# Performance work log

Measured on AMD Instinct MI355X. Metric: run time of the kernel, lower is better.

The kernel has to match this reference:

```python
import jax, jax.numpy as jnp
import numpy as np

D_MODEL = 1024
NUM_HEADS = 16
D_K = D_MODEL // NUM_HEADS


def setup_inputs() -> dict:
    key = jax.random.key(0)
    ks = jax.random.split(key, 5)
    B, S = 4, 2048
    scale = 1.0 / np.sqrt(D_MODEL)
    x = jax.random.normal(ks[0], (B, S, D_MODEL), dtype=jnp.float32)
    # Linear(d_model, d_model, bias=False) weights, stored as [out, in] like torch
    Wq = jax.random.normal(ks[1], (D_MODEL, D_MODEL), dtype=jnp.float32) * scale
    Wk = jax.random.normal(ks[2], (D_MODEL, D_MODEL), dtype=jnp.float32) * scale
    Wv = jax.random.normal(ks[3], (D_MODEL, D_MODEL), dtype=jnp.float32) * scale
    Wo = jax.random.normal(ks[4], (D_MODEL, D_MODEL), dtype=jnp.float32) * scale
    return {"x": x, "Wq": Wq, "Wk": Wk, "Wv": Wv, "Wo": Wo}


def reference(x, Wq, Wk, Wv, Wo):
    B, S, D = x.shape
    H, dk = NUM_HEADS, D_K
    # projections (torch Linear: x @ W.T)
    q = (x @ Wq.T).reshape(B, S, H, dk).transpose(0, 2, 1, 3)  # [B,H,S,dk]
    k = (x @ Wk.T).reshape(B, S, H, dk).transpose(0, 2, 1, 3)
    v = (x @ Wv.T).reshape(B, S, H, dk).transpose(0, 2, 1, 3)
    scores = jnp.einsum("bhqd,bhkd->bhqk", q, k) / jnp.sqrt(jnp.float32(dk))
    causal = jnp.triu(jnp.ones((S, S), dtype=bool), k=1)  # True above diagonal -> masked
    scores = jnp.where(causal[None, None], -jnp.inf, scores)
    attn = jax.nn.softmax(scores, axis=-1)
    out = jnp.einsum("bhqk,bhkd->bhqd", attn, v)  # [B,H,S,dk]
    out = out.transpose(0, 2, 1, 3).reshape(B, S, D)
    return out @ Wo.T
```

## Files before the change

kernel.cpp:

```cpp
#include <hip/hip_runtime.h>

typedef __bf16 bf16_t;
typedef __bf16 bf16x8 __attribute__((ext_vector_type(8)));
typedef __bf16 bf16x4 __attribute__((ext_vector_type(4)));
typedef float f32x4 __attribute__((ext_vector_type(4)));
typedef unsigned short u16x8 __attribute__((ext_vector_type(8)));

#define AS1C(p) ((const __attribute__((address_space(1))) void*)(p))
#define AS3(p) ((__attribute__((address_space(3))) void*)(p))

__device__ __forceinline__ unsigned short f2b_rne(float f) {
  union { float f; unsigned u; } x; x.f = f;
  unsigned u = x.u;
  u += 0x7fffu + ((u >> 16) & 1u);
  return (unsigned short)(u >> 16);
}

__global__ __launch_bounds__(256) void cast_f32_bf16(const float* __restrict__ in,
                                                     unsigned short* __restrict__ out,
                                                     int n) {
  int i = (blockIdx.x * 256 + threadIdx.x) * 8;
  if (i >= n) return;
  const float4* p = reinterpret_cast<const float4*>(in + i);
  float4 a = p[0], b = p[1];
  u16x8 o;
  o[0] = f2b_rne(a.x); o[1] = f2b_rne(a.y); o[2] = f2b_rne(a.z); o[3] = f2b_rne(a.w);
  o[4] = f2b_rne(b.x); o[5] = f2b_rne(b.y); o[6] = f2b_rne(b.z); o[7] = f2b_rne(b.w);
  *reinterpret_cast<u16x8*>(out + i) = o;
}

template <int OUT_F32>
__global__ __launch_bounds__(256) void gemm_bt(const bf16_t* __restrict__ A,
                                               const bf16_t* __restrict__ Bm,
                                               void* __restrict__ C,
                                               int M, int N, int K, int lda,
                                               float scale, int qlim) {
  __shared__ bf16_t As[128 * 32];
  __shared__ bf16_t Bs[128 * 32];
  const int tid = threadIdx.x;
  const int lane = tid & 63, wave = tid >> 6;
  const int wm = wave >> 1, wn = wave & 1;
  const int r = lane & 15, kg = lane >> 4;
  const int m0 = blockIdx.y * 128, n0 = blockIdx.x * 128;
  const float sc = (n0 < qlim) ? scale : 1.0f;
  f32x4 acc[4][4] = {};
  const size_t abase = (size_t)m0 * lda;
  const size_t bbase = (size_t)n0 * K;
  for (int k0 = 0; k0 < K; k0 += 32) {
#pragma unroll
    for (int c = 0; c < 2; ++c) {
      int e = (c * 256 + tid) * 8;
      int rr = e >> 5, cc = e & 31;
      __builtin_amdgcn_global_load_lds(AS1C(A + abase + (size_t)rr * lda + k0 + cc),
                                       AS3(As + (c * 256 + wave * 64) * 8), 16, 0, 0);
      __builtin_amdgcn_global_load_lds(AS1C(Bm + bbase + (size_t)rr * K + k0 + cc),
                                       AS3(Bs + (c * 256 + wave * 64) * 8), 16, 0, 0);
    }
    __syncthreads();
    bf16x8 af[4], bfr[4];
#pragma unroll
    for (int t = 0; t < 4; ++t) {
      af[t]  = *reinterpret_cast<const bf16x8*>(As + (wm * 64 + t * 16 + r) * 32 + kg * 8);
      bfr[t] = *reinterpret_cast<const bf16x8*>(Bs + (wn * 64 + t * 16 + r) * 32 + kg * 8);
    }
#pragma unroll
    for (int i = 0; i < 4; ++i)
#pragma unroll
      for (int j = 0; j < 4; ++j)
        acc[i][j] = __builtin_amdgcn_mfma_f32_16x16x32_bf16(af[i], bfr[j], acc[i][j], 0, 0, 0);
    __syncthreads();
  }
#pragma unroll
  for (int i = 0; i < 4; ++i) {
#pragma unroll
    for (int j = 0; j < 4; ++j) {
      const int mb = m0 + wm * 64 + i * 16 + kg * 4;
      const int nc = n0 + wn * 64 + j * 16 + r;
#pragma unroll
      for (int v = 0; v < 4; ++v) {
        float val = acc[i][j][v] * sc;
        size_t idx = (size_t)(mb + v) * N + nc;
        if (OUT_F32) reinterpret_cast<float*>(C)[idx] = val;
        else reinterpret_cast<unsigned short*>(C)[idx] = f2b_rne(val);
      }
    }
  }
}

__global__ __launch_bounds__(256) void transpose_v(const bf16_t* __restrict__ qkv,
                                                   bf16_t* __restrict__ vt) {
  __shared__ bf16_t Vs[64 * 72];
  const int t = threadIdx.x;
  const int s0 = blockIdx.x * 64;
  const int bh = blockIdx.y;
  const int b = bh >> 4, h = bh & 15;
  const size_t in_base = ((size_t)b * 2048 + s0) * 3072 + 2048 + h * 64;
#pragma unroll
  for (int c = 0; c < 2; ++c) {
    int chunk = c * 256 + t;
    int ss = chunk >> 3, dd = (chunk & 7) * 8;
    bf16x8 v = *reinterpret_cast<const bf16x8*>(qkv + in_base + (size_t)ss * 3072 + dd);
    *reinterpret_cast<bf16x8*>(Vs + ss * 72 + dd) = v;
  }
  __syncthreads();
  const size_t out_base = (size_t)bh * 64 * 2048 + s0;
#pragma unroll
  for (int c = 0; c < 2; ++c) {
    int chunk = c * 256 + t;
    int dd = chunk >> 3, ss = (chunk & 7) * 8;
    bf16x8 o;
#pragma unroll
    for (int j = 0; j < 8; ++j) o[j] = Vs[(ss + j) * 72 + dd];
    *reinterpret_cast<bf16x8*>(vt + out_base + (size_t)dd * 2048 + ss) = o;
  }
}

__global__ __launch_bounds__(512) void flash_attn(const bf16_t* __restrict__ QKV,
                                                  const bf16_t* __restrict__ VT,
                                                  unsigned short* __restrict__ O,
                                                  int ostride) {
  __shared__ bf16_t Ks[64 * 72];
  __shared__ bf16_t Vts[64 * 72];
  __shared__ bf16_t Pl[8][16 * 72];
  const int tid = threadIdx.x;
  const int lane = tid & 63, wave = tid >> 6;
  const int r = lane & 15, kg = lane >> 4;
  const int bh = blockIdx.y;
  const int b = bh >> 4, h = bh & 15;
  const size_t qkv_row0 = (size_t)b * 2048 * 3072;
  const int qcol = h * 64, kcol = 1024 + h * 64;
  const size_t vt_base = (size_t)bh * 64 * 2048;
  const size_t o_row0 = (size_t)b * 2048 * ostride;
  const int ocol = h * 64;
  const int srr = tid >> 3, scc = (tid & 7) * 8;

  for (int pass = 0; pass < 2; ++pass) {
    const int qt = pass ? (15 - (int)blockIdx.x) : (int)blockIdx.x;
    const int q0 = qt * 128;
    const int qrow = q0 + wave * 16 + r;
    const int tmax_w = (q0 + wave * 16 + 15) >> 6;
    const int ntiles = qt * 2 + 2;

    const size_t qoff = qkv_row0 + (size_t)qrow * 3072 + qcol;
    bf16x8 qf0 = *reinterpret_cast<const bf16x8*>(QKV + qoff + kg * 8);
    bf16x8 qf1 = *reinterpret_cast<const bf16x8*>(QKV + qoff + 32 + kg * 8);

    f32x4 oacc[4] = {};
    float m_run = -3e30f, l_run = 0.f;

    bf16x8 gk = *reinterpret_cast<const bf16x8*>(QKV + qkv_row0 + (size_t)srr * 3072 + kcol + scc);
    bf16x8 gv = *reinterpret_cast<const bf16x8*>(VT + vt_base + (size_t)srr * 2048 + scc);

    for (int t = 0; t < ntiles; ++t) {
      __syncthreads();
      *reinterpret_cast<bf16x8*>(Ks + srr * 72 + scc) = gk;
      *reinterpret_cast<bf16x8*>(Vts + srr * 72 + scc) = gv;
      __syncthreads();
      if (t + 1 < ntiles) {
        const int kv1 = (t + 1) * 64;
        gk = *reinterpret_cast<const bf16x8*>(QKV + qkv_row0 + (size_t)(kv1 + srr) * 3072 + kcol + scc);
        gv = *reinterpret_cast<const bf16x8*>(VT + vt_base + (size_t)srr * 2048 + kv1 + scc);
      }
      if (t > tmax_w) continue;

      const int kv0 = t * 64;
      float vals[16];
#pragma unroll
      for (int nt = 0; nt < 4; ++nt) {
        bf16x8 kf0 = *reinterpret_cast<const bf16x8*>(Ks + (nt * 16 + r) * 72 + kg * 8);
        bf16x8 kf1 = *reinterpret_cast<const bf16x8*>(Ks + (nt * 16 + r) * 72 + 32 + kg * 8);
        f32x4 s = {};
        s = __builtin_amdgcn_mfma_f32_16x16x32_bf16(kf0, qf0, s, 0, 0, 0);
        s = __builtin_amdgcn_mfma_f32_16x16x32_bf16(kf1, qf1, s, 0, 0, 0);
#pragma unroll
        for (int v = 0; v < 4; ++v) vals[nt * 4 + v] = s[v];
      }
      if (t == tmax_w) {
#pragma unroll
        for (int nt = 0; nt < 4; ++nt)
#pragma unroll
          for (int v = 0; v < 4; ++v)
            if (kv0 + nt * 16 + kg * 4 + v > qrow) vals[nt * 4 + v] = -3e30f;
      }
      float pmax = vals[0];
#pragma unroll
      for (int ii = 1; ii < 16; ++ii) pmax = fmaxf(pmax, vals[ii]);
      pmax = fmaxf(pmax, __shfl_xor(pmax, 16));
      pmax = fmaxf(pmax, __shfl_xor(pmax, 32));
      const float m_new = fmaxf(m_run, pmax);
      const float alpha = __expf(m_run - m_new);
      float psum = 0.f;
#pragma unroll
      for (int ii = 0; ii < 16; ++ii) {
        float p = __expf(vals[ii] - m_new);
        vals[ii] = p;
        psum += p;
      }
      psum += __shfl_xor(psum, 16);
      psum += __shfl_xor(psum, 32);
      l_run = l_run * alpha + psum;
      m_run = m_new;

#pragma unroll
      for (int nt = 0; nt < 4; ++nt) {
        bf16x4 pb;
#pragma unroll
        for (int v = 0; v < 4; ++v) pb[v] = (bf16_t)vals[nt * 4 + v];
        *reinterpret_cast<bf16x4*>(&Pl[wave][r * 72 + nt * 16 + kg * 4]) = pb;
      }
      bf16x8 pa0 = *reinterpret_cast<const bf16x8*>(&Pl[wave][r * 72 + kg * 8]);
      bf16x8 pa1 = *reinterpret_cast<const bf16x8*>(&Pl[wave][r * 72 + 32 + kg * 8]);

      f32x4 al;
#pragma unroll
      for (int v = 0; v < 4; ++v) al[v] = __shfl(alpha, kg * 4 + v);
#pragma unroll
      for (int dt = 0; dt < 4; ++dt)
#pragma unroll
        for (int v = 0; v < 4; ++v) oacc[dt][v] *= al[v];

#pragma unroll
      for (int dt = 0; dt < 4; ++dt) {
        bf16x8 vb0 = *reinterpret_cast<const bf16x8*>(Vts + (dt * 16 + r) * 72 + kg * 8);
        oacc[dt] = __builtin_amdgcn_mfma_f32_16x16x32_bf16(pa0, vb0, oacc[dt], 0, 0, 0);
        bf16x8 vb1 = *reinterpret_cast<const bf16x8*>(Vts + (dt * 16 + r) * 72 + 32 + kg * 8);
        oacc[dt] = __builtin_amdgcn_mfma_f32_16x16x32_bf16(pa1, vb1, oacc[dt], 0, 0, 0);
      }
    }

    const float linv = 1.0f / l_run;
    f32x4 il;
#pragma unroll
    for (int v = 0; v < 4; ++v) il[v] = __shfl(linv, kg * 4 + v);
    const size_t orow0 = o_row0 + (size_t)(q0 + wave * 16) * ostride + ocol;
#pragma unroll
    for (int dt = 0; dt < 4; ++dt) {
      const int d = dt * 16 + r;
#pragma unroll
      for (int v = 0; v < 4; ++v)
        O[orow0 + (size_t)(kg * 4 + v) * ostride + d] = f2b_rne(oacc[dt][v] * il[v]);
    }
  }
}

extern "C" void kernel_launch(void* const* d_in, const int* in_sizes, int n_in,
                              void* d_out, int out_size, void* d_ws, size_t ws_size,
                              hipStream_t stream) {
  const float* x  = (const float*)d_in[0];
  const float* Wq = (const float*)d_in[1];
  const float* Wk = (const float*)d_in[2];
  const float* Wv = (const float*)d_in[3];
  const float* Wo = (const float*)d_in[4];

  char* ws = (char*)d_ws;
  bf16_t* xb  = (bf16_t*)(ws);
  bf16_t* wqb = (bf16_t*)(ws + (16u << 20));
  bf16_t* wkb = (bf16_t*)(ws + (18u << 20));
  bf16_t* wvb = (bf16_t*)(ws + (20u << 20));
  bf16_t* qkv = (bf16_t*)(ws + (24u << 20));
  bf16_t* vt  = (bf16_t*)(ws);
  bf16_t* wob = (bf16_t*)(ws + (16u << 20));

  const int NX = 4 * 2048 * 1024;
  const int NW = 1024 * 1024;
  cast_f32_bf16<<<NX / 2048, 256, 0, stream>>>(x,  (unsigned short*)xb,  NX);
  cast_f32_bf16<<<NW / 2048, 256, 0, stream>>>(Wq, (unsigned short*)wqb, NW);
  cast_f32_bf16<<<NW / 2048, 256, 0, stream>>>(Wk, (unsigned short*)wkb, NW);
  cast_f32_bf16<<<NW / 2048, 256, 0, stream>>>(Wv, (unsigned short*)wvb, NW);

  gemm_bt<0><<<dim3(3072 / 128, 8192 / 128), 256, 0, stream>>>(
      xb, wqb, qkv, 8192, 3072, 1024, 1024, 0.125f, 1024);

  transpose_v<<<dim3(2048 / 64, 64), 256, 0, stream>>>(qkv, vt);

  cast_f32_bf16<<<NW / 2048, 256, 0, stream>>>(Wo, (unsigned short*)wob, NW);

  flash_attn<<<dim3(8, 64), 512, 0, stream>>>(qkv, vt, (unsigned short*)qkv, 3072);

  gemm_bt<1><<<dim3(1024 / 128, 8192 / 128), 256, 0, stream>>>(
      qkv, wob, d_out, 8192, 1024, 1024, 3072, 1.0f, 0);
}
```

Baseline: 212.0 us.

## Fuse weight casts, use exp2 softmax with lazy rescale, remap attention grid

Folds log2(e) into the Q scale so softmax can use hardware exp2, and skips the output rescale while the running max grows by no more than a threshold. Merges the four weight casts into one launch. Replaces the two-pass paired q-tile attention with one q-tile per block and an XCD-aware block-to-head mapping that schedules the longest tiles first. Adds s_setprio around the MFMA sequences in the GEMM and attention kernels. These changes target launch overhead, transcendental cost, rescale work and L2 locality, at the risk of losing the causal load balance the paired tiles provided.

```diff
diff --git a/kernel.cpp b/kernel.cpp
--- a/kernel.cpp
+++ b/kernel.cpp
@@ -14,6 +14,10 @@
   unsigned u = x.u;
   u += 0x7fffu + ((u >> 16) & 1u);
   return (unsigned short)(u >> 16);
+}
+
+__device__ __forceinline__ float fast_exp2(float x) {
+  return __builtin_amdgcn_exp2f(x);
 }
 
 __global__ __launch_bounds__(256) void cast_f32_bf16(const float* __restrict__ in,
@@ -27,6 +31,23 @@
   o[0] = f2b_rne(a.x); o[1] = f2b_rne(a.y); o[2] = f2b_rne(a.z); o[3] = f2b_rne(a.w);
   o[4] = f2b_rne(b.x); o[5] = f2b_rne(b.y); o[6] = f2b_rne(b.z); o[7] = f2b_rne(b.w);
   *reinterpret_cast<u16x8*>(out + i) = o;
+}
+
+__global__ __launch_bounds__(256) void cast_w4(const float* __restrict__ w0,
+                                               const float* __restrict__ w1,
+                                               const float* __restrict__ w2,
+                                               const float* __restrict__ w3,
+                                               unsigned short* __restrict__ out) {
+  const float* in = (blockIdx.y == 0) ? w0 : (blockIdx.y == 1) ? w1
+                  : (blockIdx.y == 2) ? w2 : w3;
+  int i = (blockIdx.x * 256 + threadIdx.x) * 8;
+  unsigned short* o = out + (size_t)blockIdx.y * (1024u * 1024u);
+  const float4* p = reinterpret_cast<const float4*>(in + i);
+  float4 a = p[0], b = p[1];
+  u16x8 v;
+  v[0] = f2b_rne(a.x); v[1] = f2b_rne(a.y); v[2] = f2b_rne(a.z); v[3] = f2b_rne(a.w);
+  v[4] = f2b_rne(b.x); v[5] = f2b_rne(b.y); v[6] = f2b_rne(b.z); v[7] = f2b_rne(b.w);
+  *reinterpret_cast<u16x8*>(o + i) = v;
 }
 
 template <int OUT_F32>
@@ -63,11 +84,13 @@
       af[t]  = *reinterpret_cast<const bf16x8*>(As + (wm * 64 + t * 16 + r) * 32 + kg * 8);
       bfr[t] = *reinterpret_cast<const bf16x8*>(Bs + (wn * 64 + t * 16 + r) * 32 + kg * 8);
     }
+    __builtin_amdgcn_s_setprio(1);
 #pragma unroll
     for (int i = 0; i < 4; ++i)
 #pragma unroll
       for (int j = 0; j < 4; ++j)
         acc[i][j] = __builtin_amdgcn_mfma_f32_16x16x32_bf16(af[i], bfr[j], acc[i][j], 0, 0, 0);
+    __builtin_amdgcn_s_setprio(0);
     __syncthreads();
   }
 #pragma unroll
@@ -125,7 +148,9 @@
   const int tid = threadIdx.x;
   const int lane = tid & 63, wave = tid >> 6;
   const int r = lane & 15, kg = lane >> 4;
-  const int bh = blockIdx.y;
+  const int xcd = blockIdx.x & 7;
+  const int bh = xcd * 8 + (blockIdx.y & 7);
+  const int qt = 15 - ((blockIdx.x >> 3) * 8 + (blockIdx.y >> 3));
   const int b = bh >> 4, h = bh & 15;
   const size_t qkv_row0 = (size_t)b * 2048 * 3072;
   const int qcol = h * 64, kcol = 1024 + h * 64;
@@ -134,112 +159,118 @@
   const int ocol = h * 64;
   const int srr = tid >> 3, scc = (tid & 7) * 8;
 
-  for (int pass = 0; pass < 2; ++pass) {
-    const int qt = pass ? (15 - (int)blockIdx.x) : (int)blockIdx.x;
-    const int q0 = qt * 128;
-    const int qrow = q0 + wave * 16 + r;
-    const int tmax_w = (q0 + wave * 16 + 15) >> 6;
-    const int ntiles = qt * 2 + 2;
-
-    const size_t qoff = qkv_row0 + (size_t)qrow * 3072 + qcol;
-    bf16x8 qf0 = *reinterpret_cast<const bf16x8*>(QKV + qoff + kg * 8);
-    bf16x8 qf1 = *reinterpret_cast<const bf16x8*>(QKV + qoff + 32 + kg * 8);
-
-    f32x4 oacc[4] = {};
-    float m_run = -3e30f, l_run = 0.f;
-
-    bf16x8 gk = *reinterpret_cast<const bf16x8*>(QKV + qkv_row0 + (size_t)srr * 3072 + kcol + scc);
-    bf16x8 gv = *reinterpret_cast<const bf16x8*>(VT + vt_base + (size_t)srr * 2048 + scc);
-
-    for (int t = 0; t < ntiles; ++t) {
-      __syncthreads();
-      *reinterpret_cast<bf16x8*>(Ks + srr * 72 + scc) = gk;
-      *reinterpret_cast<bf16x8*>(Vts + srr * 72 + scc) = gv;
-      __syncthreads();
-      if (t + 1 < ntiles) {
-        const int kv1 = (t + 1) * 64;
-        gk = *reinterpret_cast<const bf16x8*>(QKV + qkv_row0 + (size_t)(kv1 + srr) * 3072 + kcol + scc);
-        gv = *reinterpret_cast<const bf16x8*>(VT + vt_base + (size_t)srr * 2048 + kv1 + scc);
-      }
-      if (t > tmax_w) continue;
-
-      const int kv0 = t * 64;
-      float vals[16];
-#pragma unroll
-      for (int nt = 0; nt < 4; ++nt) {
-        bf16x8 kf0 = *reinterpret_cast<const bf16x8*>(Ks + (nt * 16 + r) * 72 + kg * 8);
-        bf16x8 kf1 = *reinterpret_cast<const bf16x8*>(Ks + (nt * 16 + r) * 72 + 32 + kg * 8);
-        f32x4 s = {};
-        s = __builtin_amdgcn_mfma_f32_16x16x32_bf16(kf0, qf0, s, 0, 0, 0);
-        s = __builtin_amdgcn_mfma_f32_16x16x32_bf16(kf1, qf1, s, 0, 0, 0);
-#pragma unroll
-        for (int v = 0; v < 4; ++v) vals[nt * 4 + v] = s[v];
-      }
-      if (t == tmax_w) {
-#pragma unroll
-        for (int nt = 0; nt < 4; ++nt)
-#pragma unroll
-          for (int v = 0; v < 4; ++v)
-            if (kv0 + nt * 16 + kg * 4 + v > qrow) vals[nt * 4 + v] = -3e30f;
-      }
-      float pmax = vals[0];
-#pragma unroll
-      for (int ii = 1; ii < 16; ++ii) pmax = fmaxf(pmax, vals[ii]);
-      pmax = fmaxf(pmax, __shfl_xor(pmax, 16));
-      pmax = fmaxf(pmax, __shfl_xor(pmax, 32));
+  const int q0 = qt * 128;
+  const int qrow = q0 + wave * 16 + r;
+  const int tmax_w = (q0 + wave * 16 + 15) >> 6;
+  const int ntiles = qt * 2 + 2;
+
+  const size_t qoff = qkv_row0 + (size_t)qrow * 3072 + qcol;
+  bf16x8 qf0 = *reinterpret_cast<const bf16x8*>(QKV + qoff + kg * 8);
+  bf16x8 qf1 = *reinterpret_cast<const bf16x8*>(QKV + qoff + 32 + kg * 8);
+
+  f32x4 oacc[4] = {};
+  float m_run = -3e30f, l_run = 0.f;
+
+  bf16x8 gk = *reinterpret_cast<const bf16x8*>(QKV + qkv_row0 + (size_t)srr * 3072 + kcol + scc);
+  bf16x8 gv = *reinterpret_cast<const bf16x8*>(VT + vt_base + (size_t)srr * 2048 + scc);
+
+  for (int t = 0; t < ntiles; ++t) {
+    __syncthreads();
+    *reinterpret_cast<bf16x8*>(Ks + srr * 72 + scc) = gk;
+    *reinterpret_cast<bf16x8*>(Vts + srr * 72 + scc) = gv;
+    __syncthreads();
+    if (t + 1 < ntiles) {
+      const int kv1 = (t + 1) * 64;
+      gk = *reinterpret_cast<const bf16x8*>(QKV + qkv_row0 + (size_t)(kv1 + srr) * 3072 + kcol + scc);
+      gv = *reinterpret_cast<const bf16x8*>(VT + vt_base + (size_t)srr * 2048 + kv1 + scc);
+    }
+    if (t > tmax_w) continue;
+
+    const int kv0 = t * 64;
+    float vals[16];
+#pragma unroll
+    for (int nt = 0; nt < 4; ++nt) {
+      bf16x8 kf0 = *reinterpret_cast<const bf16x8*>(Ks + (nt * 16 + r) * 72 + kg * 8);
+      bf16x8 kf1 = *reinterpret_cast<const bf16x8*>(Ks + (nt * 16 + r) * 72 + 32 + kg * 8);
+      f32x4 s = {};
+      __builtin_amdgcn_s_setprio(1);
+      s = __builtin_amdgcn_mfma_f32_16x16x32_bf16(kf0, qf0, s, 0, 0, 0);
+      s = __builtin_amdgcn_mfma_f32_16x16x32_bf16(kf1, qf1, s, 0, 0, 0);
+      __builtin_amdgcn_s_setprio(0);
+#pragma unroll
+      for (int v = 0; v < 4; ++v) vals[nt * 4 + v] = s[v];
+    }
+    if (t == tmax_w) {
+#pragma unroll
+      for (int nt = 0; nt < 4; ++nt)
+#pragma unroll
+        for (int v = 0; v < 4; ++v)
+          if (kv0 + nt * 16 + kg * 4 + v > qrow) vals[nt * 4 + v] = -3e30f;
+    }
+    float a0 = fmaxf(fmaxf(vals[0], vals[1]), vals[2]);
+    float a1 = fmaxf(fmaxf(vals[3], vals[4]), vals[5]);
+    float a2 = fmaxf(fmaxf(vals[6], vals[7]), vals[8]);
+    float a3 = fmaxf(fmaxf(vals[9], vals[10]), vals[11]);
+    float a4 = fmaxf(fmaxf(vals[12], vals[13]), vals[14]);
+    float pmax = fmaxf(fmaxf(fmaxf(a0, a1), fmaxf(a2, a3)), fmaxf(a4, vals[15]));
+    pmax = fmaxf(pmax, __shfl_xor(pmax, 16));
+    pmax = fmaxf(pmax, __shfl_xor(pmax, 32));
+    if (!__all(pmax <= m_run + 8.0f)) {
       const float m_new = fmaxf(m_run, pmax);
-      const float alpha = __expf(m_run - m_new);
-      float psum = 0.f;
-#pragma unroll
-      for (int ii = 0; ii < 16; ++ii) {
-        float p = __expf(vals[ii] - m_new);
-        vals[ii] = p;
-        psum += p;
-      }
-      psum += __shfl_xor(psum, 16);
-      psum += __shfl_xor(psum, 32);
-      l_run = l_run * alpha + psum;
+      const float alpha = fast_exp2(m_run - m_new);
+      l_run *= alpha;
+      f32x4 al;
+#pragma unroll
+      for (int v = 0; v < 4; ++v) al[v] = __shfl(alpha, kg * 4 + v);
+#pragma unroll
+      for (int dt = 0; dt < 4; ++dt)
+#pragma unroll
+        for (int v = 0; v < 4; ++v) oacc[dt][v] *= al[v];
       m_run = m_new;
-
-#pragma unroll
-      for (int nt = 0; nt < 4; ++nt) {
-        bf16x4 pb;
-#pragma unroll
-        for (int v = 0; v < 4; ++v) pb[v] = (bf16_t)vals[nt * 4 + v];
-        *reinterpret_cast<bf16x4*>(&Pl[wave][r * 72 + nt * 16 + kg * 4]) = pb;
-      }
-      bf16x8 pa0 = *reinterpret_cast<const bf16x8*>(&Pl[wave][r * 72 + kg * 8]);
-      bf16x8 pa1 = *reinterpret_cast<const bf16x8*>(&Pl[wave][r * 72 + 32 + kg * 8]);
-
-      f32x4 al;
-#pragma unroll
-      for (int v = 0; v < 4; ++v) al[v] = __shfl(alpha, kg * 4 + v);
-#pragma unroll
-      for (int dt = 0; dt < 4; ++dt)
-#pragma unroll
-        for (int v = 0; v < 4; ++v) oacc[dt][v] *= al[v];
-
-#pragma unroll
-      for (int dt = 0; dt < 4; ++dt) {
-        bf16x8 vb0 = *reinterpret_cast<const bf16x8*>(Vts + (dt * 16 + r) * 72 + kg * 8);
-        oacc[dt] = __builtin_amdgcn_mfma_f32_16x16x32_bf16(pa0, vb0, oacc[dt], 0, 0, 0);
-        bf16x8 vb1 = *reinterpret_cast<const bf16x8*>(Vts + (dt * 16 + r) * 72 + 32 + kg * 8);
-        oacc[dt] = __builtin_amdgcn_mfma_f32_16x16x32_bf16(pa1, vb1, oacc[dt], 0, 0, 0);
-      }
-    }
-
-    const float linv = 1.0f / l_run;
-    f32x4 il;
-#pragma unroll
-    for (int v = 0; v < 4; ++v) il[v] = __shfl(linv, kg * 4 + v);
-    const size_t orow0 = o_row0 + (size_t)(q0 + wave * 16) * ostride + ocol;
+    }
+    float psum = 0.f;
+#pragma unroll
+    for (int ii = 0; ii < 16; ++ii) {
+      float p = fast_exp2(vals[ii] - m_run);
+      vals[ii] = p;
+      psum += p;
+    }
+    psum += __shfl_xor(psum, 16);
+    psum += __shfl_xor(psum, 32);
+    l_run += psum;
+
+#pragma unroll
+    for (int nt = 0; nt < 4; ++nt) {
+      bf16x4 pb;
+#pragma unroll
+      for (int v = 0; v < 4; ++v) pb[v] = (bf16_t)vals[nt * 4 + v];
+      *reinterpret_cast<bf16x4*>(&Pl[wave][r * 72 + nt * 16 + kg * 4]) = pb;
+    }
+    bf16x8 pa0 = *reinterpret_cast<const bf16x8*>(&Pl[wave][r * 72 + kg * 8]);
+    bf16x8 pa1 = *reinterpret_cast<const bf16x8*>(&Pl[wave][r * 72 + 32 + kg * 8]);
+
 #pragma unroll
     for (int dt = 0; dt < 4; ++dt) {
-      const int d = dt * 16 + r;
-#pragma unroll
-      for (int v = 0; v < 4; ++v)
-        O[orow0 + (size_t)(kg * 4 + v) * ostride + d] = f2b_rne(oacc[dt][v] * il[v]);
-    }
+      bf16x8 vb0 = *reinterpret_cast<const bf16x8*>(Vts + (dt * 16 + r) * 72 + kg * 8);
+      bf16x8 vb1 = *reinterpret_cast<const bf16x8*>(Vts + (dt * 16 + r) * 72 + 32 + kg * 8);
+      __builtin_amdgcn_s_setprio(1);
+      oacc[dt] = __builtin_amdgcn_mfma_f32_16x16x32_bf16(pa0, vb0, oacc[dt], 0, 0, 0);
+      oacc[dt] = __builtin_amdgcn_mfma_f32_16x16x32_bf16(pa1, vb1, oacc[dt], 0, 0, 0);
+      __builtin_amdgcn_s_setprio(0);
+    }
+  }
+
+  const float linv = 1.0f / l_run;
+  f32x4 il;
+#pragma unroll
+  for (int v = 0; v < 4; ++v) il[v] = __shfl(linv, kg * 4 + v);
+  const size_t orow0 = o_row0 + (size_t)(q0 + wave * 16) * ostride + ocol;
+#pragma unroll
+  for (int dt = 0; dt < 4; ++dt) {
+    const int d = dt * 16 + r;
+#pragma unroll
+    for (int v = 0; v < 4; ++v)
+      O[orow0 + (size_t)(kg * 4 + v) * ostride + d] = f2b_rne(oacc[dt][v] * il[v]);
   }
 }
 
@@ -255,27 +286,20 @@
   char* ws = (char*)d_ws;
   bf16_t* xb  = (bf16_t*)(ws);
   bf16_t* wqb = (bf16_t*)(ws + (16u << 20));
-  bf16_t* wkb = (bf16_t*)(ws + (18u << 20));
-  bf16_t* wvb = (bf16_t*)(ws + (20u << 20));
+  bf16_t* wob = (bf16_t*)(ws + (22u << 20));
   bf16_t* qkv = (bf16_t*)(ws + (24u << 20));
   bf16_t* vt  = (bf16_t*)(ws);
-  bf16_t* wob = (bf16_t*)(ws + (16u << 20));
 
   const int NX = 4 * 2048 * 1024;
-  const int NW = 1024 * 1024;
-  cast_f32_bf16<<<NX / 2048, 256, 0, stream>>>(x,  (unsigned short*)xb,  NX);
-  cast_f32_bf16<<<NW / 2048, 256, 0, stream>>>(Wq, (unsigned short*)wqb, NW);
-  cast_f32_bf16<<<NW / 2048, 256, 0, stream>>>(Wk, (unsigned short*)wkb, NW);
-  cast_f32_bf16<<<NW / 2048, 256, 0, stream>>>(Wv, (unsigned short*)wvb, NW);
+  cast_f32_bf16<<<NX / 2048, 256, 0, stream>>>(x, (unsigned short*)xb, NX);
+  cast_w4<<<dim3(512, 4), 256, 0, stream>>>(Wq, Wk, Wv, Wo, (unsigned short*)wqb);
 
   gemm_bt<0><<<dim3(3072 / 128, 8192 / 128), 256, 0, stream>>>(
-      xb, wqb, qkv, 8192, 3072, 1024, 1024, 0.125f, 1024);
+      xb, wqb, qkv, 8192, 3072, 1024, 1024, 0.18033688011112042f, 1024);
 
   transpose_v<<<dim3(2048 / 64, 64), 256, 0, stream>>>(qkv, vt);
 
-  cast_f32_bf16<<<NW / 2048, 256, 0, stream>>>(Wo, (unsigned short*)wob, NW);
-
-  flash_attn<<<dim3(8, 64), 512, 0, stream>>>(qkv, vt, (unsigned short*)qkv, 3072);
+  flash_attn<<<dim3(16, 64), 512, 0, stream>>>(qkv, vt, (unsigned short*)qkv, 3072);
 
   gemm_bt<1><<<dim3(1024 / 128, 8192 / 128), 256, 0, stream>>>(
       qkv, wob, d_out, 8192, 1024, 1024, 3072, 1.0f, 0);
```

Measured after the change: 213.9 us. About the same (+0.9%).
